# Kernel tuning notes

Measured on AMD Instinct MI355X. Metric: run time of the kernel, lower is better.

Reference implementation:

```python
import jax, jax.numpy as jnp
import numpy as np

B, S, D = 2, 2048, 1024
N_QK, N_V, N_KNOW = 4096, 4096, 8192
N_HEADS = 16
MAX_K_QK, MAX_K_V, MAX_K_KNOW = 32, 32, 64
LN_EPS = 1e-6


def _unit_norm(key, shape, scale=1.0):
    x = jax.random.normal(key, shape, jnp.float32)
    return x / (jnp.linalg.norm(x, axis=-1, keepdims=True) + 1e-8) * scale


def setup_inputs() -> dict:
    key = jax.random.key(0)
    ks = jax.random.split(key, 12)
    return {
        "x": jax.random.normal(ks[0], (B, S, D), jnp.float32),
        "qk_emb": _unit_norm(ks[1], (N_QK, D)),
        "qk_w": _unit_norm(ks[2], (N_QK, D)),
        "v_emb": _unit_norm(ks[3], (N_V, D)),
        "v_w": _unit_norm(ks[4], (N_V, D)),
        "know_emb": _unit_norm(ks[5], (N_KNOW, D)),
        "know_w": _unit_norm(ks[6], (N_KNOW, D)),
        "tau_attn_k": jax.random.normal(ks[7], (D, 3), jnp.float32) * (1.0 / np.sqrt(D)),
        "tau_attn_b": jnp.zeros((3,), jnp.float32),
        "tau_know_k": jax.random.normal(ks[8], (D, 1), jnp.float32) * (1.0 / np.sqrt(D)),
        "tau_know_b": jnp.zeros((1,), jnp.float32),
        "expand_O": jax.random.normal(ks[9], (D, D), jnp.float32) * 0.02,
        "ln1_scale": jnp.ones((D,), jnp.float32),
        "ln1_bias": jnp.zeros((D,), jnp.float32),
        "ln2_scale": jnp.ones((D,), jnp.float32),
        "ln2_bias": jnp.zeros((D,), jnp.float32),
    }


def _layer_norm(x, scale, bias):
    mean = jnp.mean(x, axis=-1, keepdims=True)
    var = jnp.mean(jnp.square(x - mean), axis=-1, keepdims=True)
    return (x - mean) / jnp.sqrt(var + LN_EPS) * scale + bias


def threshold_gate(scores, tau, max_k):
    # scores: [B,S,N], tau: [B,S,1]
    raw = scores - tau
    gate = jnp.where(raw > 0, raw, 1e-8 * jnp.exp(raw))
    exp_gate = jnp.exp(gate) - 1.0
    topk_vals, _ = jax.lax.top_k(exp_gate, min(max_k, scores.shape[-1]))
    thr = topk_vals[:, :, -1:]
    exp_gate = jnp.where(exp_gate >= thr, exp_gate, 0.0)
    gate_sum = exp_gate.sum(axis=-1, keepdims=True) + 1e-8
    strength = jnp.tanh(exp_gate.max(axis=-1, keepdims=True))
    return exp_gate / gate_sum * strength


@jax.checkpoint
def sense_emit_full(x, emb, w, gate):
    # [B,S,D] @ [D,N] -> gated [B,S,N] -> [B,S,D]
    return ((x @ emb.T) * gate) @ w


def _block(x, qk_emb, qk_w, v_emb, v_w, know_emb, know_w,
           tau_attn_k, tau_attn_b, tau_know_k, tau_know_b,
           expand_O, ln1_scale, ln1_bias, ln2_scale, ln2_bias):
    # ---- attention circuit (deterministic; dropout = identity) ----
    normed = _layer_norm(x, ln1_scale, ln1_bias)
    scores_qk = normed @ qk_emb.T           # [B,S,N_QK]
    scores_v = normed @ v_emb.T             # [B,S,N_V]
    tau_all = normed @ tau_attn_k + tau_attn_b  # [B,S,3]
    g_Q = threshold_gate(scores_qk, tau_all[:, :, 0:1], MAX_K_QK)
    g_K = threshold_gate(scores_qk, tau_all[:, :, 1:2], MAX_K_QK)
    g_V = threshold_gate(scores_v, tau_all[:, :, 2:3], MAX_K_V)
    t_qk = 1.0 / qk_emb.shape[0]
    t_v = 1.0 / v_emb.shape[0]
    a_aux = (((g_Q.mean(axis=(0, 1)) - t_qk) ** 2).sum() * g_Q.shape[-1]
             + ((g_K.mean(axis=(0, 1)) - t_qk) ** 2).sum() * g_K.shape[-1]
             + ((g_V.mean(axis=(0, 1)) - t_v) ** 2).sum() * g_V.shape[-1])

    Q = sense_emit_full(normed, qk_emb, qk_w, g_Q)
    K = sense_emit_full(normed, qk_emb, qk_w, g_K)
    V = sense_emit_full(normed, v_emb, v_w, g_V)

    Bs, Ss, Ds = x.shape
    d_head = Ds // N_HEADS
    Q = Q.reshape(Bs, Ss, N_HEADS, d_head).transpose(0, 2, 1, 3)
    K = K.reshape(Bs, Ss, N_HEADS, d_head).transpose(0, 2, 1, 3)
    V = V.reshape(Bs, Ss, N_HEADS, d_head).transpose(0, 2, 1, 3)
    scale = jnp.sqrt(jnp.float32(d_head))
    attn = jnp.einsum('bhsd,bhtd->bhst', Q, K) / scale
    causal = jnp.tril(jnp.ones((Ss, Ss), dtype=jnp.bool_))
    attn = jnp.where(causal, attn, jnp.finfo(attn.dtype).min)
    attn = jax.nn.softmax(attn, axis=-1)
    out = jnp.einsum('bhst,bhtd->bhsd', attn, V)
    out = out.transpose(0, 2, 1, 3).reshape(Bs, Ss, Ds)
    out = out @ expand_O
    x = x + out

    # ---- knowledge circuit ----
    normed = _layer_norm(x, ln2_scale, ln2_bias)
    scores_k = normed @ know_emb.T          # [B,S,N_KNOW]
    tau_k = normed @ tau_know_k + tau_know_b
    gate = threshold_gate(scores_k, tau_k, MAX_K_KNOW)
    t_k = 1.0 / know_emb.shape[0]
    k_aux = ((gate.mean(axis=(0, 1)) - t_k) ** 2).sum() * know_emb.shape[0]
    know_out = sense_emit_full(normed, know_emb, know_w, gate)
    x = x + know_out
    return x, a_aux + k_aux


def reference(x, qk_emb, qk_w, v_emb, v_w, know_emb, know_w,
              tau_attn_k, tau_attn_b, tau_know_k, tau_know_b,
              expand_O, ln1_scale, ln1_bias, ln2_scale, ln2_bias):
    return _block(x, qk_emb, qk_w, v_emb, v_w, know_emb, know_w,
                  tau_attn_k, tau_attn_b, tau_know_k, tau_know_b,
                  expand_O, ln1_scale, ln1_bias, ln2_scale, ln2_bias)
```

## Files before the change

### kernel.cpp

```cpp
#include <hip/hip_runtime.h>

#define TOK   4096
#define DIM   1024
#define NQK   4096
#define NV    4096
#define NKN   8192
#define SLEN  2048
#define NH    16
#define DH    64
#define CAPA  48
#define CAPK  96
#define APAD  72

typedef float  f32x4  __attribute__((ext_vector_type(4)));
typedef short  short8 __attribute__((ext_vector_type(8)));
typedef unsigned int  u32;
typedef unsigned short u16;

__device__ __forceinline__ u16 f2bf(float f) {
    u32 u = __float_as_uint(f);
    u32 r = (u + 0x7fffu + ((u >> 16) & 1u)) >> 16;
    return (u16)r;
}
__device__ __forceinline__ float bf2f(u16 v) { return __uint_as_float(((u32)v) << 16); }

__device__ __forceinline__ u16 bfkey(u16 b) {
    return (b & 0x8000u) ? (u16)(~b) : (u16)(b | 0x8000u);
}
__device__ __forceinline__ u16 keybf(u16 k) {
    return (k & 0x8000u) ? (u16)(k & 0x7fffu) : (u16)(~k);
}

__device__ __forceinline__ f32x4 mfma_bf16(short8 a, short8 b, f32x4 c) {
    asm volatile("v_mfma_f32_16x16x32_bf16 %0, %1, %2, %0"
                 : "+v"(c) : "v"(a), "v"(b));
    return c;
}

__device__ __forceinline__ void gload16(const u16* g, u16* s) {
    __builtin_amdgcn_global_load_lds((const __attribute__((address_space(1))) void*)g,
                                     (__attribute__((address_space(3))) void*)s, 16, 0, 0);
}

__device__ __forceinline__ float blockReduceF(float v, float* red, int wave, int lane) {
#pragma unroll
    for (int off = 32; off > 0; off >>= 1) v += __shfl_xor(v, off);
    __syncthreads();
    if (lane == 0) red[wave] = v;
    __syncthreads();
    return red[0] + red[1] + red[2] + red[3];
}

__global__ __launch_bounds__(256) void k_convert_all(const float* __restrict__ p0,
                                                     const float* __restrict__ p1,
                                                     const float* __restrict__ p2,
                                                     const float* __restrict__ p3,
                                                     const float* __restrict__ p4,
                                                     const float* __restrict__ p5,
                                                     u16* __restrict__ o0, u16* __restrict__ o1,
                                                     u16* __restrict__ o2, u16* __restrict__ o3,
                                                     u16* __restrict__ o4, u16* __restrict__ o5) {
    const int S0 = 1048576, S1 = 2097152, S2 = 4194304, S3 = 5242880, S4 = 6291456, S5 = 8388608;
    for (int i = blockIdx.x * 256 + threadIdx.x; i < S5; i += gridDim.x * 256) {
        const float* in; u16* out; int off;
        if (i < S0)      { in = p0; out = o0; off = i; }
        else if (i < S1) { in = p1; out = o1; off = i - S0; }
        else if (i < S2) { in = p2; out = o2; off = i - S1; }
        else if (i < S3) { in = p3; out = o3; off = i - S2; }
        else if (i < S4) { in = p4; out = o4; off = i - S3; }
        else             { in = p5; out = o5; off = i - S4; }
        float4 v = reinterpret_cast<const float4*>(in)[off];
        reinterpret_cast<ushort4*>(out)[off] = make_ushort4(f2bf(v.x), f2bf(v.y), f2bf(v.z), f2bf(v.w));
    }
}

__global__ __launch_bounds__(256) void k_transpose_bf16(const float* __restrict__ in,
                                                        u16* __restrict__ out) {
    __shared__ float tile[32][33];
    int bx = blockIdx.x * 32;
    int by = blockIdx.y * 32;
    int tx = threadIdx.x & 31;
    int ty = threadIdx.x >> 5;
    for (int r = ty; r < 32; r += 8)
        tile[r][tx] = in[(size_t)(by + r) * DIM + bx + tx];
    __syncthreads();
    for (int r = ty; r < 32; r += 8)
        out[(size_t)(bx + r) * DIM + by + tx] = f2bf(tile[tx][r]);
}

__global__ __launch_bounds__(256) void k_ln_tau(const float* __restrict__ x,
                                                const float* __restrict__ sc,
                                                const float* __restrict__ bi,
                                                const float* __restrict__ tauk,
                                                const float* __restrict__ taub,
                                                int ntau,
                                                u16* __restrict__ nrm,
                                                float* __restrict__ tau_out) {
    __shared__ float red[4];
    int t = blockIdx.x, tid = threadIdx.x, wave = tid >> 6, lane = tid & 63;
    const float4 xv = reinterpret_cast<const float4*>(x + (size_t)t * DIM)[tid];
    float s = xv.x + xv.y + xv.z + xv.w;
    s = blockReduceF(s, red, wave, lane);
    float mean = s * (1.0f / DIM);
    float d0 = xv.x - mean, d1 = xv.y - mean, d2 = xv.z - mean, d3 = xv.w - mean;
    float ss = d0 * d0 + d1 * d1 + d2 * d2 + d3 * d3;
    ss = blockReduceF(ss, red, wave, lane);
    float rstd = rsqrtf(ss * (1.0f / DIM) + 1e-6f);
    const float4 scv = reinterpret_cast<const float4*>(sc)[tid];
    const float4 biv = reinterpret_cast<const float4*>(bi)[tid];
    float n0 = d0 * rstd * scv.x + biv.x;
    float n1 = d1 * rstd * scv.y + biv.y;
    float n2 = d2 * rstd * scv.z + biv.z;
    float n3 = d3 * rstd * scv.w + biv.w;
    ushort4 o = make_ushort4(f2bf(n0), f2bf(n1), f2bf(n2), f2bf(n3));
    reinterpret_cast<ushort4*>(nrm + (size_t)t * DIM)[tid] = o;
    int d = tid * 4;
    for (int j = 0; j < ntau; j++) {
        float p = n0 * tauk[(size_t)(d + 0) * ntau + j] + n1 * tauk[(size_t)(d + 1) * ntau + j]
                + n2 * tauk[(size_t)(d + 2) * ntau + j] + n3 * tauk[(size_t)(d + 3) * ntau + j];
        p = blockReduceF(p, red, wave, lane);
        if (tid == 0) tau_out[(size_t)t * ntau + j] = p + taub[j];
    }
}

template<int TAG, int KEYOUT>
__global__ __launch_bounds__(256) void k_gemm_bt(const u16* __restrict__ A,
                                                 const u16* __restrict__ B,
                                                 void* __restrict__ Cv,
                                                 int M, int N, int K,
                                                 const float* __restrict__ res) {
    __shared__ __align__(16) u16 As[4096];
    __shared__ __align__(16) u16 Bs[4096];
    int tid = threadIdx.x;
    int wave = tid >> 6, lane = tid & 63;
    int m0 = blockIdx.y * 128, n0 = blockIdx.x * 128;
    int wm = (wave >> 1) * 64, wn = (wave & 1) * 64;
    int kg = lane >> 4, l15 = lane & 15;

    const u16* gA0 = A + (size_t)(m0 + lane) * K + wave * 8;
    const u16* gA1 = A + (size_t)(m0 + 64 + lane) * K + wave * 8;
    const u16* gB0 = B + (size_t)(n0 + lane) * K + wave * 8;
    const u16* gB1 = B + (size_t)(n0 + 64 + lane) * K + wave * 8;
    u16* sA0 = As + wave * 1024;
    u16* sA1 = As + wave * 1024 + 512;
    u16* sB0 = Bs + wave * 1024;
    u16* sB1 = Bs + wave * 1024 + 512;

    f32x4 acc[4][4];
#pragma unroll
    for (int i = 0; i < 4; i++)
#pragma unroll
        for (int j = 0; j < 4; j++) { f32x4 z = {0.f, 0.f, 0.f, 0.f}; acc[i][j] = z; }

    for (int k0 = 0; k0 < K; k0 += 32) {
        __syncthreads();
        gload16(gA0 + k0, sA0);
        gload16(gA1 + k0, sA1);
        gload16(gB0 + k0, sB0);
        gload16(gB1 + k0, sB1);
        __syncthreads();
        short8 af[4], bg[4];
#pragma unroll
        for (int mi = 0; mi < 4; mi++) {
            int row = wm + mi * 16 + l15;
            af[mi] = *reinterpret_cast<const short8*>(&As[(kg * 128 + row) * 8]);
        }
#pragma unroll
        for (int ni = 0; ni < 4; ni++) {
            int row = wn + ni * 16 + l15;
            bg[ni] = *reinterpret_cast<const short8*>(&Bs[(kg * 128 + row) * 8]);
        }
#pragma unroll
        for (int mi = 0; mi < 4; mi++)
#pragma unroll
            for (int ni = 0; ni < 4; ni++)
                acc[mi][ni] = mfma_bf16(af[mi], bg[ni], acc[mi][ni]);
    }
    asm volatile("s_nop 7\n\ts_nop 7");
#pragma unroll
    for (int mi = 0; mi < 4; mi++) {
#pragma unroll
        for (int ni = 0; ni < 4; ni++) {
            int col = n0 + wn + ni * 16 + l15;
#pragma unroll
            for (int r = 0; r < 4; r++) {
                int rowm = m0 + wm + mi * 16 + (lane >> 4) * 4 + r;
                size_t idx = (size_t)rowm * N + col;
                float v = acc[mi][ni][r];
                if (KEYOUT) {
                    ((u16*)Cv)[idx] = bfkey(f2bf(v));
                } else {
                    if (res) v += res[idx];
                    ((float*)Cv)[idx] = v;
                }
            }
        }
    }
}

template<int TWO, int RES>
__global__ __launch_bounds__(256) void k_gate_emit(const u16* __restrict__ keys_g, int NC, int ksel,
                                                   int row_off,
                                                   const float* __restrict__ tau, int tau_stride, int tcol0,
                                                   const u16* __restrict__ w,
                                                   u16* __restrict__ OA, u16* __restrict__ OB,
                                                   float* __restrict__ io,
                                                   float* __restrict__ csA, float* __restrict__ csB) {
    extern __shared__ u16 keys[];
    __shared__ int   hist[256];
    __shared__ int   scnt;
    __shared__ int   dsel;
    __shared__ int   knext;
    __shared__ int   sidx[CAPK];
    __shared__ float svA[CAPK];
    __shared__ float svB[CAPK];
    int r = blockIdx.x, tid = threadIdx.x, wave = tid >> 6, lane = tid & 63;
    int t = row_off + r;
    const int cap = TWO ? CAPA : (RES ? CAPK : CAPA);

    const uint4* srow8 = reinterpret_cast<const uint4*>(keys_g + (size_t)r * NC);
    for (int c = tid; c < NC / 8; c += 256)
        reinterpret_cast<uint4*>(keys)[c] = srow8[c];
    if (tid == 0) scnt = 0;

    u32 prefix = 0;
    int krem = ksel;
#pragma unroll
    for (int pass = 0; pass < 2; pass++) {
        int shift = 8 - pass * 8;
        hist[tid] = 0;
        __syncthreads();
        u32 pmask = (pass == 0) ? 0u : 0xFF00u;
        for (int i = tid; i < NC; i += 256) {
            u32 ky = keys[i];
            if ((ky & pmask) == prefix)
                atomicAdd(&hist[(ky >> shift) & 255], 1);
        }
        __syncthreads();
        int v = hist[tid];
#pragma unroll
        for (int off = 1; off < 256; off <<= 1) {
            int other = (tid + off < 256) ? hist[tid + off] : 0;
            __syncthreads();
            v += other;
            hist[tid] = v;
            __syncthreads();
        }
        int sfx = v;
        int sfx_next = (tid < 255) ? hist[tid + 1] : 0;
        if (sfx >= krem && (tid == 255 || sfx_next < krem)) {
            dsel = tid;
            knext = krem - sfx_next;
        }
        __syncthreads();
        prefix |= ((u32)dsel) << shift;
        krem = knext;
        __syncthreads();
    }
    u32 thr = prefix;

    for (int i = tid; i < NC; i += 256) {
        u32 ky = keys[i];
        if (ky >= thr) {
            int p = atomicAdd(&scnt, 1);
            if (p < cap) {
                sidx[p] = i;
                svA[p] = bf2f(keybf((u16)ky));
            }
        }
    }
    __syncthreads();
    int n = scnt < cap ? scnt : cap;

    if (wave == 0) {
        float tA = tau[(size_t)t * tau_stride + tcol0];
        float tB = TWO ? tau[(size_t)t * tau_stride + tcol0 + 1] : 0.f;
        float sumA = 0.f, mxA = -1e30f, sumB = 0.f, mxB = -1e30f;
        float sv0 = (lane < n) ? svA[lane] : 0.f;
        float sv1 = (lane + 64 < n) ? svA[lane + 64] : 0.f;
        for (int i = lane; i < n; i += 64) {
            float sv = svA[i];
            float rA = sv - tA;
            float gA = rA > 0.f ? rA : 1e-8f * expf(rA);
            float eA = expf(gA) - 1.0f;
            sumA += eA; mxA = fmaxf(mxA, eA);
            if (TWO) {
                float rB = sv - tB;
                float gB = rB > 0.f ? rB : 1e-8f * expf(rB);
                float eB = expf(gB) - 1.0f;
                sumB += eB; mxB = fmaxf(mxB, eB);
            }
        }
#pragma unroll
        for (int off = 32; off > 0; off >>= 1) {
            sumA += __shfl_xor(sumA, off); mxA = fmaxf(mxA, __shfl_xor(mxA, off));
            sumB += __shfl_xor(sumB, off); mxB = fmaxf(mxB, __shfl_xor(mxB, off));
        }
        float fA = tanhf(mxA) / (sumA + 1e-8f);
        float fB = tanhf(mxB) / (sumB + 1e-8f);
        if (lane < n) {
            float sv = sv0; int ci = sidx[lane];
            float rA = sv - tA;
            float gA = rA > 0.f ? rA : 1e-8f * expf(rA);
            float ga = (expf(gA) - 1.0f) * fA;
            svA[lane] = ga * sv;
            atomicAdd(&csA[ci], ga);
            if (TWO) {
                float rB = sv - tB;
                float gB = rB > 0.f ? rB : 1e-8f * expf(rB);
                float gb = (expf(gB) - 1.0f) * fB;
                svB[lane] = gb * sv;
                atomicAdd(&csB[ci], gb);
            }
        }
        if (lane + 64 < n) {
            float sv = sv1; int ci = sidx[lane + 64];
            float rA = sv - tA;
            float gA = rA > 0.f ? rA : 1e-8f * expf(rA);
            float ga = (expf(gA) - 1.0f) * fA;
            svA[lane + 64] = ga * sv;
            atomicAdd(&csA[ci], ga);
            if (TWO) {
                float rB = sv - tB;
                float gB = rB > 0.f ? rB : 1e-8f * expf(rB);
                float gb = (expf(gB) - 1.0f) * fB;
                svB[lane + 64] = gb * sv;
                atomicAdd(&csB[ci], gb);
            }
        }
    }
    __syncthreads();

    float a0 = 0, a1 = 0, a2 = 0, a3 = 0, b0 = 0, b1 = 0, b2 = 0, b3 = 0;
    float4 base;
    if (RES) base = reinterpret_cast<const float4*>(io + (size_t)t * DIM)[tid];
    int s = 0;
    for (; s + 4 <= n; s += 4) {
        const ushort4 w0 = reinterpret_cast<const ushort4*>(w + (size_t)sidx[s]     * DIM)[tid];
        const ushort4 w1 = reinterpret_cast<const ushort4*>(w + (size_t)sidx[s + 1] * DIM)[tid];
        const ushort4 w2 = reinterpret_cast<const ushort4*>(w + (size_t)sidx[s + 2] * DIM)[tid];
        const ushort4 w3 = reinterpret_cast<const ushort4*>(w + (size_t)sidx[s + 3] * DIM)[tid];
        float vA0 = svA[s], vA1 = svA[s + 1], vA2 = svA[s + 2], vA3 = svA[s + 3];
        a0 += vA0 * bf2f(w0.x) + vA1 * bf2f(w1.x) + vA2 * bf2f(w2.x) + vA3 * bf2f(w3.x);
        a1 += vA0 * bf2f(w0.y) + vA1 * bf2f(w1.y) + vA2 * bf2f(w2.y) + vA3 * bf2f(w3.y);
        a2 += vA0 * bf2f(w0.z) + vA1 * bf2f(w1.z) + vA2 * bf2f(w2.z) + vA3 * bf2f(w3.z);
        a3 += vA0 * bf2f(w0.w) + vA1 * bf2f(w1.w) + vA2 * bf2f(w2.w) + vA3 * bf2f(w3.w);
        if (TWO) {
            float vB0 = svB[s], vB1 = svB[s + 1], vB2 = svB[s + 2], vB3 = svB[s + 3];
            b0 += vB0 * bf2f(w0.x) + vB1 * bf2f(w1.x) + vB2 * bf2f(w2.x) + vB3 * bf2f(w3.x);
            b1 += vB0 * bf2f(w0.y) + vB1 * bf2f(w1.y) + vB2 * bf2f(w2.y) + vB3 * bf2f(w3.y);
            b2 += vB0 * bf2f(w0.z) + vB1 * bf2f(w1.z) + vB2 * bf2f(w2.z) + vB3 * bf2f(w3.z);
            b3 += vB0 * bf2f(w0.w) + vB1 * bf2f(w1.w) + vB2 * bf2f(w2.w) + vB3 * bf2f(w3.w);
        }
    }
    for (; s < n; s++) {
        const ushort4 wv = reinterpret_cast<const ushort4*>(w + (size_t)sidx[s] * DIM)[tid];
        float va = svA[s];
        a0 += va * bf2f(wv.x); a1 += va * bf2f(wv.y); a2 += va * bf2f(wv.z); a3 += va * bf2f(wv.w);
        if (TWO) {
            float vb = svB[s];
            b0 += vb * bf2f(wv.x); b1 += vb * bf2f(wv.y); b2 += vb * bf2f(wv.z); b3 += vb * bf2f(wv.w);
        }
    }
    if (RES) {
        reinterpret_cast<float4*>(io + (size_t)t * DIM)[tid] =
            make_float4(base.x + a0, base.y + a1, base.z + a2, base.w + a3);
    } else {
        reinterpret_cast<ushort4*>(OA + (size_t)t * DIM)[tid] = make_ushort4(f2bf(a0), f2bf(a1), f2bf(a2), f2bf(a3));
        if (TWO)
            reinterpret_cast<ushort4*>(OB + (size_t)t * DIM)[tid] = make_ushort4(f2bf(b0), f2bf(b1), f2bf(b2), f2bf(b3));
    }
}

__global__ __launch_bounds__(256) void k_attn(const u16* __restrict__ Q,
                                              const u16* __restrict__ K,
                                              const u16* __restrict__ V,
                                              u16* __restrict__ O) {
    __shared__ __align__(16) u16 Qs[64 * APAD];
    __shared__ __align__(16) u16 Ks[64 * APAD];
    __shared__ __align__(16) u16 Vt[64 * APAD];
    __shared__ __align__(16) u16 Ps[4][16 * APAD];
    int tid = threadIdx.x, wave = tid >> 6, lane = tid & 63;
    int h = blockIdx.x, bb = blockIdx.y, qt = blockIdx.z;
    int q0 = qt * 64;
    size_t base = ((size_t)bb * SLEN) * DIM + (size_t)h * DH;
    int sr = tid >> 2, sc = (tid & 3) * 16;
    int g = lane >> 4, l15 = lane & 15;

    {
        const u16* qp = Q + base + (size_t)(q0 + sr) * DIM + sc;
        *reinterpret_cast<short8*>(&Qs[sr * APAD + sc])     = *reinterpret_cast<const short8*>(qp);
        *reinterpret_cast<short8*>(&Qs[sr * APAD + sc + 8]) = *reinterpret_cast<const short8*>(qp + 8);
    }
    __syncthreads();
    short8 qa0 = *reinterpret_cast<const short8*>(&Qs[(wave * 16 + l15) * APAD + g * 8]);
    short8 qa1 = *reinterpret_cast<const short8*>(&Qs[(wave * 16 + l15) * APAD + 32 + g * 8]);

    float m[4], l[4];
    f32x4 oacc[4];
#pragma unroll
    for (int i = 0; i < 4; i++) {
        m[i] = -1e30f; l[i] = 0.f;
        f32x4 z = {0.f, 0.f, 0.f, 0.f}; oacc[i] = z;
    }
    u16* pw = &Ps[wave][0];

    for (int kc = 0; kc <= qt; kc++) {
        __syncthreads();
        {
            const u16* kp = K + base + (size_t)(kc * 64 + sr) * DIM + sc;
            *reinterpret_cast<short8*>(&Ks[sr * APAD + sc])     = *reinterpret_cast<const short8*>(kp);
            *reinterpret_cast<short8*>(&Ks[sr * APAD + sc + 8]) = *reinterpret_cast<const short8*>(kp + 8);
            const u16* vp = V + base + (size_t)(kc * 64 + sr) * DIM + sc;
            short8 w0 = *reinterpret_cast<const short8*>(vp);
            short8 w1 = *reinterpret_cast<const short8*>(vp + 8);
            const u16* w0p = reinterpret_cast<const u16*>(&w0);
            const u16* w1p = reinterpret_cast<const u16*>(&w1);
#pragma unroll
            for (int j = 0; j < 16; j++) {
                int d = sc + j;
                int phys = (((sr >> 3) + d + (d >> 4)) & 7);
                Vt[d * APAD + phys * 8 + (sr & 7)] = (j < 8) ? w0p[j] : w1p[j - 8];
            }
        }
        __syncthreads();

        f32x4 s4[4];
#pragma unroll
        for (int ks = 0; ks < 4; ks++) {
            f32x4 z = {0.f, 0.f, 0.f, 0.f}; s4[ks] = z;
            short8 kb0 = *reinterpret_cast<const short8*>(&Ks[(ks * 16 + l15) * APAD + g * 8]);
            short8 kb1 = *reinterpret_cast<const short8*>(&Ks[(ks * 16 + l15) * APAD + 32 + g * 8]);
            s4[ks] = mfma_bf16(qa0, kb0, s4[ks]);
            s4[ks] = mfma_bf16(qa1, kb1, s4[ks]);
        }
        asm volatile("s_nop 7\n\ts_nop 7");

        int key_base = kc * 64 + l15;
#pragma unroll
        for (int ks = 0; ks < 4; ks++) {
            int key = key_base + ks * 16;
#pragma unroll
            for (int r = 0; r < 4; r++) {
                int q_abs = q0 + wave * 16 + g * 4 + r;
                float sv = s4[ks][r] * 0.125f;
                s4[ks][r] = (key > q_abs) ? -1e30f : sv;
            }
        }

#pragma unroll
        for (int r = 0; r < 4; r++) {
            float mx = fmaxf(fmaxf(s4[0][r], s4[1][r]), fmaxf(s4[2][r], s4[3][r]));
            mx = fmaxf(mx, __shfl_xor(mx, 1));
            mx = fmaxf(mx, __shfl_xor(mx, 2));
            mx = fmaxf(mx, __shfl_xor(mx, 4));
            mx = fmaxf(mx, __shfl_xor(mx, 8));
            float mnew = fmaxf(m[r], mx);
            float al = __expf(m[r] - mnew);
            m[r] = mnew;
            float p0 = __expf(s4[0][r] - mnew);
            float p1 = __expf(s4[1][r] - mnew);
            float p2 = __expf(s4[2][r] - mnew);
            float p3 = __expf(s4[3][r] - mnew);
            float ps = p0 + p1 + p2 + p3;
            ps += __shfl_xor(ps, 1);
            ps += __shfl_xor(ps, 2);
            ps += __shfl_xor(ps, 4);
            ps += __shfl_xor(ps, 8);
            l[r] = l[r] * al + ps;
#pragma unroll
            for (int ds_ = 0; ds_ < 4; ds_++) oacc[ds_][r] *= al;
            int row = g * 4 + r;
            pw[row * APAD +  0 + l15] = f2bf(p0);
            pw[row * APAD + 16 + l15] = f2bf(p1);
            pw[row * APAD + 32 + l15] = f2bf(p2);
            pw[row * APAD + 48 + l15] = f2bf(p3);
        }

        short8 pa0 = *reinterpret_cast<const short8*>(&pw[l15 * APAD + g * 8]);
        short8 pa1 = *reinterpret_cast<const short8*>(&pw[l15 * APAD + 32 + g * 8]);
#pragma unroll
        for (int dsub = 0; dsub < 4; dsub++) {
            int d = dsub * 16 + l15;
            int rot = d + (d >> 4);
            short8 vb0 = *reinterpret_cast<const short8*>(&Vt[d * APAD + (((0 + g) + rot) & 7) * 8]);
            short8 vb1 = *reinterpret_cast<const short8*>(&Vt[d * APAD + (((4 + g) + rot) & 7) * 8]);
            oacc[dsub] = mfma_bf16(pa0, vb0, oacc[dsub]);
            oacc[dsub] = mfma_bf16(pa1, vb1, oacc[dsub]);
        }
    }
    asm volatile("s_nop 7\n\ts_nop 7");

#pragma unroll
    for (int r = 0; r < 4; r++) {
        float inv = 1.0f / l[r];
        int row = q0 + wave * 16 + g * 4 + r;
#pragma unroll
        for (int dsub = 0; dsub < 4; dsub++) {
            O[base + (size_t)row * DIM + dsub * 16 + l15] = f2bf(oacc[dsub][r] * inv);
        }
    }
}

__global__ __launch_bounds__(256) void k_aux(const float* __restrict__ cs,
                                             float* __restrict__ out_aux) {
    __shared__ float red[4];
    int gtid = blockIdx.x * 256 + threadIdx.x;
    float acc = 0.f;
    for (int i = gtid; i < 3 * 4096 + 8192; i += gridDim.x * 256) {
        float mean = cs[i] * (1.0f / 4096.0f);
        float tN, Nf;
        if (i < 12288) { tN = 1.0f / 4096.0f; Nf = 4096.0f; }
        else           { tN = 1.0f / 8192.0f; Nf = 8192.0f; }
        float d = mean - tN;
        acc += d * d * Nf;
    }
    acc = blockReduceF(acc, red, threadIdx.x >> 6, threadIdx.x & 63);
    if (threadIdx.x == 0) atomicAdd(out_aux, acc);
}

extern "C" void kernel_launch(void* const* d_in, const int* in_sizes, int n_in,
                              void* d_out, int out_size, void* d_ws, size_t ws_size,
                              hipStream_t stream) {
    const float* x         = (const float*)d_in[0];
    const float* qk_emb    = (const float*)d_in[1];
    const float* qk_w      = (const float*)d_in[2];
    const float* v_emb     = (const float*)d_in[3];
    const float* v_w       = (const float*)d_in[4];
    const float* know_emb  = (const float*)d_in[5];
    const float* know_w    = (const float*)d_in[6];
    const float* tau_attn_k = (const float*)d_in[7];
    const float* tau_attn_b = (const float*)d_in[8];
    const float* tau_know_k = (const float*)d_in[9];
    const float* tau_know_b = (const float*)d_in[10];
    const float* expand_O  = (const float*)d_in[11];
    const float* ln1_s     = (const float*)d_in[12];
    const float* ln1_b     = (const float*)d_in[13];
    const float* ln2_s     = (const float*)d_in[14];
    const float* ln2_b     = (const float*)d_in[15];
    float* out = (float*)d_out;
    char*  ws  = (char*)d_ws;

    u16*   nrm_bf   = (u16*)(ws + 0);
    u16*   qkemb_bf = (u16*)(ws + 8388608);
    u16*   vemb_bf  = (u16*)(ws + 16777216);
    u16*   knemb_bf = (u16*)(ws + 25165824);
    u16*   expT_bf  = (u16*)(ws + 41943040);
    u16*   attn_bf  = (u16*)(ws + 44040192);
    u16*   qkw_bf   = (u16*)(ws + 52428800);
    u16*   vw_bf    = (u16*)(ws + 60817408);
    u16*   knw_bf   = (u16*)(ws + 69206016);
    u16*   Qb       = (u16*)(ws + 85983232);
    u16*   Kb       = (u16*)(ws + 94371840);
    u16*   Vb       = (u16*)(ws + 102760448);
    u16*   keysbuf  = (u16*)(ws + 111149056);
    float* tauA     = (float*)(ws + 185384960);
    float* tauKn    = (float*)(ws + 185434112);
    float* colsum   = (float*)(ws + 185450496);
    const size_t WS_NEEDED = 185532416;
    if (ws_size < WS_NEEDED) return;

    float* colQ = colsum, *colK = colsum + 4096, *colV = colsum + 8192, *colKn = colsum + 12288;

    hipMemsetAsync(colsum, 0, 20480 * sizeof(float), stream);
    hipMemsetAsync(out + (size_t)TOK * DIM, 0, sizeof(float), stream);

    k_convert_all<<<2048, 256, 0, stream>>>(qk_emb, v_emb, know_emb, qk_w, v_w, know_w,
                                            qkemb_bf, vemb_bf, knemb_bf, qkw_bf, vw_bf, knw_bf);
    k_transpose_bf16<<<dim3(32, 32), 256, 0, stream>>>(expand_O, expT_bf);

    k_ln_tau<<<TOK, 256, 0, stream>>>(x, ln1_s, ln1_b, tau_attn_k, tau_attn_b, 3, nrm_bf, tauA);

    k_gemm_bt<0, 1><<<dim3(NQK / 128, TOK / 128), 256, 0, stream>>>(nrm_bf, qkemb_bf, keysbuf, TOK, NQK, DIM, nullptr);
    k_gate_emit<1, 0><<<TOK, 256, NQK * sizeof(u16), stream>>>(keysbuf, NQK, 32, 0, tauA, 3, 0,
                                                               qkw_bf, Qb, Kb, nullptr, colQ, colK);
    k_gemm_bt<1, 1><<<dim3(NV / 128, TOK / 128), 256, 0, stream>>>(nrm_bf, vemb_bf, keysbuf, TOK, NV, DIM, nullptr);
    k_gate_emit<0, 0><<<TOK, 256, NV * sizeof(u16), stream>>>(keysbuf, NV, 32, 0, tauA, 3, 2,
                                                              vw_bf, Vb, nullptr, nullptr, colV, nullptr);

    k_attn<<<dim3(NH, 2, SLEN / 64), 256, 0, stream>>>(Qb, Kb, Vb, attn_bf);

    k_gemm_bt<2, 0><<<dim3(DIM / 128, TOK / 128), 256, 0, stream>>>(attn_bf, expT_bf, out, TOK, DIM, DIM, x);

    k_ln_tau<<<TOK, 256, 0, stream>>>(out, ln2_s, ln2_b, tau_know_k, tau_know_b, 1, nrm_bf, tauKn);

    for (int c = 0; c < 2; c++) {
        k_gemm_bt<3, 1><<<dim3(NKN / 128, 2048 / 128), 256, 0, stream>>>(
            nrm_bf + (size_t)c * 2048 * DIM, knemb_bf, keysbuf, 2048, NKN, DIM, nullptr);
        k_gate_emit<0, 1><<<2048, 256, NKN * sizeof(u16), stream>>>(keysbuf, NKN, 64, c * 2048, tauKn, 1, 0,
                                                                    knw_bf, nullptr, nullptr, out, colKn, nullptr);
    }

    k_aux<<<20, 256, 0, stream>>>(colsum, out + (size_t)TOK * DIM);
}
```

Measured before the change: 743.9 us.

## Double-buffer LDS tiles in bf16 GEMM and merge knowledge-circuit chunk launches

The bf16 GEMM kernel now keeps two LDS buffers for the A and B tiles. It prefetches the next K-slice into the spare buffer while running MFMAs on the current one, which removes one barrier per iteration and lets global loads overlap compute. The knowledge-circuit GEMM and gate/emit, which ran as two 2048-token chunks, now run as a single launch over all tokens. That single launch needs the score buffer to hold the full token-by-NKN key matrix. The change doubles GEMM shared-memory use, which may lower occupancy.

```diff
diff --git a/kernel.cpp b/kernel.cpp
--- a/kernel.cpp
+++ b/kernel.cpp
@@ -129,8 +129,8 @@
                                                  void* __restrict__ Cv,
                                                  int M, int N, int K,
                                                  const float* __restrict__ res) {
-    __shared__ __align__(16) u16 As[4096];
-    __shared__ __align__(16) u16 Bs[4096];
+    __shared__ __align__(16) u16 As[2][4096];
+    __shared__ __align__(16) u16 Bs[2][4096];
     int tid = threadIdx.x;
     int wave = tid >> 6, lane = tid & 63;
     int m0 = blockIdx.y * 128, n0 = blockIdx.x * 128;
@@ -141,10 +141,6 @@
     const u16* gA1 = A + (size_t)(m0 + 64 + lane) * K + wave * 8;
     const u16* gB0 = B + (size_t)(n0 + lane) * K + wave * 8;
     const u16* gB1 = B + (size_t)(n0 + 64 + lane) * K + wave * 8;
-    u16* sA0 = As + wave * 1024;
-    u16* sA1 = As + wave * 1024 + 512;
-    u16* sB0 = Bs + wave * 1024;
-    u16* sB1 = Bs + wave * 1024 + 512;
 
     f32x4 acc[4][4];
 #pragma unroll
@@ -152,29 +148,40 @@
 #pragma unroll
         for (int j = 0; j < 4; j++) { f32x4 z = {0.f, 0.f, 0.f, 0.f}; acc[i][j] = z; }
 
+    gload16(gA0, As[0] + wave * 1024);
+    gload16(gA1, As[0] + wave * 1024 + 512);
+    gload16(gB0, Bs[0] + wave * 1024);
+    gload16(gB1, Bs[0] + wave * 1024 + 512);
+
+    int cur = 0;
     for (int k0 = 0; k0 < K; k0 += 32) {
         __syncthreads();
-        gload16(gA0 + k0, sA0);
-        gload16(gA1 + k0, sA1);
-        gload16(gB0 + k0, sB0);
-        gload16(gB1 + k0, sB1);
-        __syncthreads();
+        if (k0 + 32 < K) {
+            int kn = k0 + 32;
+            gload16(gA0 + kn, As[cur ^ 1] + wave * 1024);
+            gload16(gA1 + kn, As[cur ^ 1] + wave * 1024 + 512);
+            gload16(gB0 + kn, Bs[cur ^ 1] + wave * 1024);
+            gload16(gB1 + kn, Bs[cur ^ 1] + wave * 1024 + 512);
+        }
+        const u16* Ac = As[cur];
+        const u16* Bc = Bs[cur];
         short8 af[4], bg[4];
 #pragma unroll
         for (int mi = 0; mi < 4; mi++) {
             int row = wm + mi * 16 + l15;
-            af[mi] = *reinterpret_cast<const short8*>(&As[(kg * 128 + row) * 8]);
+            af[mi] = *reinterpret_cast<const short8*>(&Ac[(kg * 128 + row) * 8]);
         }
 #pragma unroll
         for (int ni = 0; ni < 4; ni++) {
             int row = wn + ni * 16 + l15;
-            bg[ni] = *reinterpret_cast<const short8*>(&Bs[(kg * 128 + row) * 8]);
+            bg[ni] = *reinterpret_cast<const short8*>(&Bc[(kg * 128 + row) * 8]);
         }
 #pragma unroll
         for (int mi = 0; mi < 4; mi++)
 #pragma unroll
             for (int ni = 0; ni < 4; ni++)
                 acc[mi][ni] = mfma_bf16(af[mi], bg[ni], acc[mi][ni]);
+        cur ^= 1;
     }
     asm volatile("s_nop 7\n\ts_nop 7");
 #pragma unroll
@@ -584,12 +591,9 @@
 
     k_ln_tau<<<TOK, 256, 0, stream>>>(out, ln2_s, ln2_b, tau_know_k, tau_know_b, 1, nrm_bf, tauKn);
 
-    for (int c = 0; c < 2; c++) {
-        k_gemm_bt<3, 1><<<dim3(NKN / 128, 2048 / 128), 256, 0, stream>>>(
-            nrm_bf + (size_t)c * 2048 * DIM, knemb_bf, keysbuf, 2048, NKN, DIM, nullptr);
-        k_gate_emit<0, 1><<<2048, 256, NKN * sizeof(u16), stream>>>(keysbuf, NKN, 64, c * 2048, tauKn, 1, 0,
-                                                                    knw_bf, nullptr, nullptr, out, colKn, nullptr);
-    }
+    k_gemm_bt<3, 1><<<dim3(NKN / 128, TOK / 128), 256, 0, stream>>>(nrm_bf, knemb_bf, keysbuf, TOK, NKN, DIM, nullptr);
+    k_gate_emit<0, 1><<<TOK, 256, NKN * sizeof(u16), stream>>>(keysbuf, NKN, 64, 0, tauKn, 1, 0,
+                                                               knw_bf, nullptr, nullptr, out, colKn, nullptr);
 
     k_aux<<<20, 256, 0, stream>>>(colsum, out + (size_t)TOK * DIM);
 }
```

Measured after the change: 719.8 us. 1.03x faster.

## Double GEMM K-step and merge score GEMMs into larger single launches

Applied to the files above, without the earlier changes.

The bf16 GEMM now stages a 64-wide K slice per iteration instead of 32, using 32 KB of shared memory. That halves the number of barrier pairs per tile. The QK and V score GEMMs become one GEMM with N=8192, and the gate kernels read their halves through a new row-stride argument. The two knowledge-circuit chunks also collapse into one full-token GEMM plus one gate launch. This relies on the QK and V embedding buffers being contiguous in the workspace and on the key buffer being large enough. The larger shared-memory footprint may reduce occupancy.

```diff
diff --git a/kernel.cpp b/kernel.cpp
--- a/kernel.cpp
+++ b/kernel.cpp
@@ -129,22 +129,25 @@
                                                  void* __restrict__ Cv,
                                                  int M, int N, int K,
                                                  const float* __restrict__ res) {
-    __shared__ __align__(16) u16 As[4096];
-    __shared__ __align__(16) u16 Bs[4096];
+    __shared__ __align__(16) u16 As[8192];
+    __shared__ __align__(16) u16 Bs[8192];
     int tid = threadIdx.x;
     int wave = tid >> 6, lane = tid & 63;
     int m0 = blockIdx.y * 128, n0 = blockIdx.x * 128;
     int wm = (wave >> 1) * 64, wn = (wave & 1) * 64;
     int kg = lane >> 4, l15 = lane & 15;
 
-    const u16* gA0 = A + (size_t)(m0 + lane) * K + wave * 8;
-    const u16* gA1 = A + (size_t)(m0 + 64 + lane) * K + wave * 8;
-    const u16* gB0 = B + (size_t)(n0 + lane) * K + wave * 8;
-    const u16* gB1 = B + (size_t)(n0 + 64 + lane) * K + wave * 8;
-    u16* sA0 = As + wave * 1024;
-    u16* sA1 = As + wave * 1024 + 512;
-    u16* sB0 = Bs + wave * 1024;
-    u16* sB1 = Bs + wave * 1024 + 512;
+    const u16* gA[4]; const u16* gB[4];
+    u16* sA[4]; u16* sB[4];
+#pragma unroll
+    for (int i = 0; i < 4; i++) {
+        int c = wave * 4 + i;
+        int cs = c >> 1, h = c & 1;
+        gA[i] = A + (size_t)(m0 + h * 64 + lane) * K + cs * 8;
+        gB[i] = B + (size_t)(n0 + h * 64 + lane) * K + cs * 8;
+        sA[i] = As + cs * 1024 + h * 512;
+        sB[i] = Bs + cs * 1024 + h * 512;
+    }
 
     f32x4 acc[4][4];
 #pragma unroll
@@ -152,29 +155,30 @@
 #pragma unroll
         for (int j = 0; j < 4; j++) { f32x4 z = {0.f, 0.f, 0.f, 0.f}; acc[i][j] = z; }
 
-    for (int k0 = 0; k0 < K; k0 += 32) {
-        __syncthreads();
-        gload16(gA0 + k0, sA0);
-        gload16(gA1 + k0, sA1);
-        gload16(gB0 + k0, sB0);
-        gload16(gB1 + k0, sB1);
-        __syncthreads();
-        short8 af[4], bg[4];
-#pragma unroll
-        for (int mi = 0; mi < 4; mi++) {
-            int row = wm + mi * 16 + l15;
-            af[mi] = *reinterpret_cast<const short8*>(&As[(kg * 128 + row) * 8]);
-        }
-#pragma unroll
-        for (int ni = 0; ni < 4; ni++) {
-            int row = wn + ni * 16 + l15;
-            bg[ni] = *reinterpret_cast<const short8*>(&Bs[(kg * 128 + row) * 8]);
-        }
-#pragma unroll
-        for (int mi = 0; mi < 4; mi++)
+    for (int k0 = 0; k0 < K; k0 += 64) {
+        __syncthreads();
+#pragma unroll
+        for (int i = 0; i < 4; i++) {
+            gload16(gA[i] + k0, sA[i]);
+            gload16(gB[i] + k0, sB[i]);
+        }
+        __syncthreads();
+#pragma unroll
+        for (int ks = 0; ks < 2; ks++) {
+            int cso = (ks * 4 + kg) * 1024;
+            short8 af[4], bg[4];
+#pragma unroll
+            for (int mi = 0; mi < 4; mi++)
+                af[mi] = *reinterpret_cast<const short8*>(&As[cso + (wm + mi * 16 + l15) * 8]);
 #pragma unroll
             for (int ni = 0; ni < 4; ni++)
-                acc[mi][ni] = mfma_bf16(af[mi], bg[ni], acc[mi][ni]);
+                bg[ni] = *reinterpret_cast<const short8*>(&Bs[cso + (wn + ni * 16 + l15) * 8]);
+#pragma unroll
+            for (int mi = 0; mi < 4; mi++)
+#pragma unroll
+                for (int ni = 0; ni < 4; ni++)
+                    acc[mi][ni] = mfma_bf16(af[mi], bg[ni], acc[mi][ni]);
+        }
     }
     asm volatile("s_nop 7\n\ts_nop 7");
 #pragma unroll
@@ -199,8 +203,8 @@
 }
 
 template<int TWO, int RES>
-__global__ __launch_bounds__(256) void k_gate_emit(const u16* __restrict__ keys_g, int NC, int ksel,
-                                                   int row_off,
+__global__ __launch_bounds__(256) void k_gate_emit(const u16* __restrict__ keys_g, int ldk,
+                                                   int NC, int ksel, int row_off,
                                                    const float* __restrict__ tau, int tau_stride, int tcol0,
                                                    const u16* __restrict__ w,
                                                    u16* __restrict__ OA, u16* __restrict__ OB,
@@ -218,7 +222,7 @@
     int t = row_off + r;
     const int cap = TWO ? CAPA : (RES ? CAPK : CAPA);
 
-    const uint4* srow8 = reinterpret_cast<const uint4*>(keys_g + (size_t)r * NC);
+    const uint4* srow8 = reinterpret_cast<const uint4*>(keys_g + (size_t)r * ldk);
     for (int c = tid; c < NC / 8; c += 256)
         reinterpret_cast<uint4*>(keys)[c] = srow8[c];
     if (tid == 0) scnt = 0;
@@ -571,11 +575,10 @@
 
     k_ln_tau<<<TOK, 256, 0, stream>>>(x, ln1_s, ln1_b, tau_attn_k, tau_attn_b, 3, nrm_bf, tauA);
 
-    k_gemm_bt<0, 1><<<dim3(NQK / 128, TOK / 128), 256, 0, stream>>>(nrm_bf, qkemb_bf, keysbuf, TOK, NQK, DIM, nullptr);
-    k_gate_emit<1, 0><<<TOK, 256, NQK * sizeof(u16), stream>>>(keysbuf, NQK, 32, 0, tauA, 3, 0,
+    k_gemm_bt<0, 1><<<dim3(8192 / 128, TOK / 128), 256, 0, stream>>>(nrm_bf, qkemb_bf, keysbuf, TOK, 8192, DIM, nullptr);
+    k_gate_emit<1, 0><<<TOK, 256, NQK * sizeof(u16), stream>>>(keysbuf, 8192, NQK, 32, 0, tauA, 3, 0,
                                                                qkw_bf, Qb, Kb, nullptr, colQ, colK);
-    k_gemm_bt<1, 1><<<dim3(NV / 128, TOK / 128), 256, 0, stream>>>(nrm_bf, vemb_bf, keysbuf, TOK, NV, DIM, nullptr);
-    k_gate_emit<0, 0><<<TOK, 256, NV * sizeof(u16), stream>>>(keysbuf, NV, 32, 0, tauA, 3, 2,
+    k_gate_emit<0, 0><<<TOK, 256, NV * sizeof(u16), stream>>>(keysbuf + 4096, 8192, NV, 32, 0, tauA, 3, 2,
                                                               vw_bf, Vb, nullptr, nullptr, colV, nullptr);
 
     k_attn<<<dim3(NH, 2, SLEN / 64), 256, 0, stream>>>(Qb, Kb, Vb, attn_bf);
@@ -584,12 +587,9 @@
 
     k_ln_tau<<<TOK, 256, 0, stream>>>(out, ln2_s, ln2_b, tau_know_k, tau_know_b, 1, nrm_bf, tauKn);
 
-    for (int c = 0; c < 2; c++) {
-        k_gemm_bt<3, 1><<<dim3(NKN / 128, 2048 / 128), 256, 0, stream>>>(
-            nrm_bf + (size_t)c * 2048 * DIM, knemb_bf, keysbuf, 2048, NKN, DIM, nullptr);
-        k_gate_emit<0, 1><<<2048, 256, NKN * sizeof(u16), stream>>>(keysbuf, NKN, 64, c * 2048, tauKn, 1, 0,
-                                                                    knw_bf, nullptr, nullptr, out, colKn, nullptr);
-    }
+    k_gemm_bt<3, 1><<<dim3(NKN / 128, TOK / 128), 256, 0, stream>>>(nrm_bf, knemb_bf, keysbuf, TOK, NKN, DIM, nullptr);
+    k_gate_emit<0, 1><<<TOK, 256, NKN * sizeof(u16), stream>>>(keysbuf, NKN, NKN, 64, 0, tauKn, 1, 0,
+                                                               knw_bf, nullptr, nullptr, out, colKn, nullptr);
 
     k_aux<<<20, 256, 0, stream>>>(colsum, out + (size_t)TOK * DIM);
 }
```

After: 715.1 us. 1.04x faster.
